# Optimization experiments

Hardware: AMD Instinct MI355X
Metric: run time of the kernel (lower is better)

Reference implementation:

```python
import jax, jax.numpy as jnp
import numpy as np

N_NODES = 50000
N_EDGES = 640000
DIM_IN = 128
DIM_OUT = 128
NUM_GRAPHS = 64


def setup_inputs() -> dict:
    key = jax.random.key(0)
    ks = jax.random.split(key, 8)
    x = jax.random.normal(ks[0], (N_NODES, DIM_IN), dtype=jnp.float32)
    edge_index = jax.random.randint(ks[1], (2, N_EDGES), 0, N_NODES, dtype=jnp.int32)
    batch = jnp.sort(jax.random.randint(ks[2], (N_NODES,), 0, NUM_GRAPHS, dtype=jnp.int32))
    s = 1.0 / np.sqrt(DIM_IN)
    W1 = jax.random.normal(ks[3], (DIM_IN, DIM_IN), dtype=jnp.float32) * s
    W2 = jax.random.normal(ks[4], (DIM_IN, DIM_IN), dtype=jnp.float32) * s
    Wlin = jax.random.normal(ks[5], (DIM_IN, DIM_OUT), dtype=jnp.float32) * s
    b1 = jnp.zeros((DIM_IN,), jnp.float32)
    b2 = jnp.zeros((DIM_IN,), jnp.float32)
    blin = jnp.zeros((DIM_OUT,), jnp.float32)
    return {"x": x, "edge_index": edge_index, "batch": batch,
            "W1": W1, "b1": b1, "W2": W2, "b2": b2, "Wlin": Wlin, "blin": blin}


def _gcn_conv(x, W, b, src, dst, n_nodes):
    # GCNConv: symmetric norm with self-loops: D^{-1/2}(A+I)D^{-1/2} X W + b
    h = x @ W                                                   # [N, d]
    deg = jax.ops.segment_sum(jnp.ones_like(dst, jnp.float32), dst,
                              num_segments=n_nodes) + 1.0       # +1 self loop
    dinv = jax.lax.rsqrt(deg)                                   # [N]
    w = dinv[src] * dinv[dst]                                   # per-edge norm [E]
    agg = jax.ops.segment_sum(h[src] * w[:, None], dst, num_segments=n_nodes)
    return agg + h * (dinv * dinv)[:, None] + b                 # self-loop term + bias


def reference(x, edge_index, batch, W1, b1, W2, b2, Wlin, blin):
    n = x.shape[0]
    src, dst = edge_index[0], edge_index[1]
    h = jax.nn.relu(_gcn_conv(x, W1, b1, src, dst, n))          # dropout = identity (eval)
    h = _gcn_conv(h, W2, b2, src, dst, n)
    # global mean pool over graphs
    s = jax.ops.segment_sum(h, batch, num_segments=NUM_GRAPHS)  # [G, d]
    cnt = jax.ops.segment_sum(jnp.ones((n,), jnp.float32), batch, num_segments=NUM_GRAPHS)
    pooled = s / jnp.maximum(cnt, 1.0)[:, None]
    return jax.nn.relu(pooled @ Wlin + blin)
```

## Files before the change

kernel.cpp:

```cpp
#include <hip/hip_runtime.h>

#define N_NODES   50000
#define N_EDGES   640000
#define DIM       128
#define NUM_GRAPHS 64
#define SLOTS     64
#define GEMM1_BLOCKS 196
#define FILL_BLOCKS  157

typedef __attribute__((ext_vector_type(8))) short          s16x8;
typedef __attribute__((ext_vector_type(8))) unsigned short u16x8;
typedef __attribute__((ext_vector_type(4))) float          f32x4;

__device__ inline float bf2f(unsigned short u) {
    unsigned v = ((unsigned)u) << 16;
    float f;
    __builtin_memcpy(&f, &v, 4);
    return f;
}
__device__ inline unsigned short f2bf(float f) {
    unsigned u;
    __builtin_memcpy(&u, &f, 4);
    u = (u + 0x7fffu + ((u >> 16) & 1u)) >> 16;
    return (unsigned short)u;
}

__global__ __launch_bounds__(128) void k_prep_w(const float* __restrict__ W1,
                                                const float* __restrict__ W2,
                                                unsigned short* __restrict__ Wt1,
                                                unsigned short* __restrict__ Wt2,
                                                int* __restrict__ cnt,
                                                float* __restrict__ pooled) {
    int k = blockIdx.x & 127;
    const float*    W  = (blockIdx.x < DIM) ? W1 : W2;
    unsigned short* Wt = (blockIdx.x < DIM) ? Wt1 : Wt2;
    int n = threadIdx.x;
    Wt[n * DIM + k] = f2bf(W[k * DIM + n]);

    int gid = blockIdx.x * 128 + threadIdx.x;
    for (int i = gid; i < N_NODES; i += 32768) cnt[i] = 0;
    if (gid < NUM_GRAPHS * DIM) pooled[gid] = 0.f;
}

__global__ __launch_bounds__(512) void k_fill_gemm1(const int* __restrict__ src,
                                                    const int* __restrict__ dst,
                                                    int* __restrict__ cnt,
                                                    unsigned short* __restrict__ slots,
                                                    const float* __restrict__ x,
                                                    const unsigned short* __restrict__ Wt1,
                                                    unsigned short* __restrict__ H1) {
    __shared__ unsigned short wsh[DIM][136];
    const int tid = threadIdx.x;

    if (blockIdx.x >= GEMM1_BLOCKS) {
        int e0 = (((blockIdx.x - GEMM1_BLOCKS) * 512) + tid) * 8;
        #pragma unroll
        for (int h = 0; h < 2; h++) {
            int e = e0 + h * 4;
            if (e + 3 < N_EDGES) {
                int4 s4 = *reinterpret_cast<const int4*>(src + e);
                int4 d4 = *reinterpret_cast<const int4*>(dst + e);
                int p0 = atomicAdd(&cnt[d4.x], 1);
                int p1 = atomicAdd(&cnt[d4.y], 1);
                int p2 = atomicAdd(&cnt[d4.z], 1);
                int p3 = atomicAdd(&cnt[d4.w], 1);
                if (p0 < SLOTS) slots[d4.x * SLOTS + p0] = (unsigned short)s4.x;
                if (p1 < SLOTS) slots[d4.y * SLOTS + p1] = (unsigned short)s4.y;
                if (p2 < SLOTS) slots[d4.z * SLOTS + p2] = (unsigned short)s4.z;
                if (p3 < SLOTS) slots[d4.w * SLOTS + p3] = (unsigned short)s4.w;
            } else if (e < N_EDGES) {
                for (int q = e; q < N_EDGES; q++) {
                    int s = src[q], d = dst[q];
                    int p = atomicAdd(&cnt[d], 1);
                    if (p < SLOTS) slots[d * SLOTS + p] = (unsigned short)s;
                }
            }
        }
        return;
    }

    #pragma unroll
    for (int i = 0; i < 4; i++) {
        int off = tid * 8 + i * 4096;
        int r = off >> 7, cc = off & 127;
        u16x8 v = *reinterpret_cast<const u16x8*>(Wt1 + off);
        *reinterpret_cast<u16x8*>(&wsh[r][cc]) = v;
    }
    __syncthreads();

    const int wid  = tid >> 6;
    const int lane = tid & 63;
    const int l15  = lane & 15;
    const int lk   = lane >> 4;
    const int row0 = blockIdx.x * 256 + wid * 32;

    f32x4 acc[2][8];
    #pragma unroll
    for (int a = 0; a < 2; a++)
        #pragma unroll
        for (int n = 0; n < 8; n++) acc[a][n] = (f32x4){0.f, 0.f, 0.f, 0.f};

    const long long r0 = min(row0 + l15,      N_NODES - 1);
    const long long r1 = min(row0 + 16 + l15, N_NODES - 1);

    #pragma unroll
    for (int kk = 0; kk < 4; kk++) {
        const int kb = kk * 32 + lk * 8;
        s16x8 a0, a1;
        const float4 p0 = *reinterpret_cast<const float4*>(x + r0 * DIM + kb);
        const float4 q0 = *reinterpret_cast<const float4*>(x + r0 * DIM + kb + 4);
        const float4 p1 = *reinterpret_cast<const float4*>(x + r1 * DIM + kb);
        const float4 q1 = *reinterpret_cast<const float4*>(x + r1 * DIM + kb + 4);
        a0[0]=(short)f2bf(p0.x); a0[1]=(short)f2bf(p0.y); a0[2]=(short)f2bf(p0.z); a0[3]=(short)f2bf(p0.w);
        a0[4]=(short)f2bf(q0.x); a0[5]=(short)f2bf(q0.y); a0[6]=(short)f2bf(q0.z); a0[7]=(short)f2bf(q0.w);
        a1[0]=(short)f2bf(p1.x); a1[1]=(short)f2bf(p1.y); a1[2]=(short)f2bf(p1.z); a1[3]=(short)f2bf(p1.w);
        a1[4]=(short)f2bf(q1.x); a1[5]=(short)f2bf(q1.y); a1[6]=(short)f2bf(q1.z); a1[7]=(short)f2bf(q1.w);
        #pragma unroll
        for (int n = 0; n < 8; n++) {
            s16x8 b = *reinterpret_cast<const s16x8*>(&wsh[n * 16 + l15][kb]);
            acc[0][n] = __builtin_amdgcn_mfma_f32_16x16x32_bf16(a0, b, acc[0][n], 0, 0, 0);
            acc[1][n] = __builtin_amdgcn_mfma_f32_16x16x32_bf16(a1, b, acc[1][n], 0, 0, 0);
        }
    }

    #pragma unroll
    for (int rh = 0; rh < 2; rh++) {
        #pragma unroll
        for (int j = 0; j < 4; j++) {
            int row = row0 + rh * 16 + lk * 4 + j;
            if (row < N_NODES) {
                #pragma unroll
                for (int n = 0; n < 8; n++)
                    H1[(long long)row * DIM + n * 16 + l15] = f2bf(acc[rh][n][j]);
            }
        }
    }
}

__global__ __launch_bounds__(512) void k_gemm2(const unsigned short* __restrict__ Ab,
                                               const unsigned short* __restrict__ Wt,
                                               unsigned short* __restrict__ H) {
    __shared__ unsigned short wsh[DIM][136];
    const int tid = threadIdx.x;

    #pragma unroll
    for (int i = 0; i < 4; i++) {
        int off = tid * 8 + i * 4096;
        int r = off >> 7, cc = off & 127;
        u16x8 v = *reinterpret_cast<const u16x8*>(Wt + off);
        *reinterpret_cast<u16x8*>(&wsh[r][cc]) = v;
    }
    __syncthreads();

    const int wid  = tid >> 6;
    const int lane = tid & 63;
    const int l15  = lane & 15;
    const int lk   = lane >> 4;
    const int row0 = blockIdx.x * 256 + wid * 32;

    f32x4 acc[2][8];
    #pragma unroll
    for (int a = 0; a < 2; a++)
        #pragma unroll
        for (int n = 0; n < 8; n++) acc[a][n] = (f32x4){0.f, 0.f, 0.f, 0.f};

    const long long r0 = min(row0 + l15,      N_NODES - 1);
    const long long r1 = min(row0 + 16 + l15, N_NODES - 1);

    #pragma unroll
    for (int kk = 0; kk < 4; kk++) {
        const int kb = kk * 32 + lk * 8;
        s16x8 a0 = *reinterpret_cast<const s16x8*>(Ab + r0 * DIM + kb);
        s16x8 a1 = *reinterpret_cast<const s16x8*>(Ab + r1 * DIM + kb);
        #pragma unroll
        for (int n = 0; n < 8; n++) {
            s16x8 b = *reinterpret_cast<const s16x8*>(&wsh[n * 16 + l15][kb]);
            acc[0][n] = __builtin_amdgcn_mfma_f32_16x16x32_bf16(a0, b, acc[0][n], 0, 0, 0);
            acc[1][n] = __builtin_amdgcn_mfma_f32_16x16x32_bf16(a1, b, acc[1][n], 0, 0, 0);
        }
    }

    #pragma unroll
    for (int rh = 0; rh < 2; rh++) {
        #pragma unroll
        for (int j = 0; j < 4; j++) {
            int row = row0 + rh * 16 + lk * 4 + j;
            if (row < N_NODES) {
                #pragma unroll
                for (int n = 0; n < 8; n++)
                    H[(long long)row * DIM + n * 16 + l15] = f2bf(acc[rh][n][j]);
            }
        }
    }
}

__device__ inline void gather_node(const int* __restrict__ cnt,
                                   const unsigned short* __restrict__ slots,
                                   const unsigned short* __restrict__ h,
                                   const float* __restrict__ bias,
                                   int n, int c, float dn, float* acc) {
    float d2 = dn * dn;
    u16x8 hv = *reinterpret_cast<const u16x8*>(h + (size_t)n * DIM + c);
    #pragma unroll
    for (int j = 0; j < 8; j++) acc[j] = bf2f(hv[j]) * d2 + bias[c + j];

    const int m = min(cnt[n], SLOTS);
    const unsigned short* sl = slots + (size_t)n * SLOTS;

    int i = 0;
    for (; i + 3 < m; i += 4) {
        int s0 = sl[i], s1 = sl[i + 1], s2 = sl[i + 2], s3 = sl[i + 3];
        float w0 = rsqrtf((float)cnt[s0] + 1.0f) * dn;
        float w1 = rsqrtf((float)cnt[s1] + 1.0f) * dn;
        float w2 = rsqrtf((float)cnt[s2] + 1.0f) * dn;
        float w3 = rsqrtf((float)cnt[s3] + 1.0f) * dn;
        u16x8 v0 = *reinterpret_cast<const u16x8*>(h + (size_t)s0 * DIM + c);
        u16x8 v1 = *reinterpret_cast<const u16x8*>(h + (size_t)s1 * DIM + c);
        u16x8 v2 = *reinterpret_cast<const u16x8*>(h + (size_t)s2 * DIM + c);
        u16x8 v3 = *reinterpret_cast<const u16x8*>(h + (size_t)s3 * DIM + c);
        #pragma unroll
        for (int j = 0; j < 8; j++)
            acc[j] += (bf2f(v0[j]) * w0 + bf2f(v1[j]) * w1) +
                      (bf2f(v2[j]) * w2 + bf2f(v3[j]) * w3);
    }
    for (; i < m; i++) {
        int s0 = sl[i];
        float w0 = rsqrtf((float)cnt[s0] + 1.0f) * dn;
        u16x8 v0 = *reinterpret_cast<const u16x8*>(h + (size_t)s0 * DIM + c);
        #pragma unroll
        for (int j = 0; j < 8; j++) acc[j] += bf2f(v0[j]) * w0;
    }
}

__global__ __launch_bounds__(256) void k_pull1(const int* __restrict__ cnt,
                                               const unsigned short* __restrict__ slots,
                                               const unsigned short* __restrict__ h,
                                               const float* __restrict__ bias,
                                               unsigned short* __restrict__ outp) {
    int gid = blockIdx.x * blockDim.x + threadIdx.x;
    int n = gid >> 4;
    if (n >= N_NODES) return;
    int c = (gid & 15) << 3;

    float dn = rsqrtf((float)cnt[n] + 1.0f);
    float acc[8];
    gather_node(cnt, slots, h, bias, n, c, dn, acc);

    u16x8 o;
    #pragma unroll
    for (int j = 0; j < 8; j++) o[j] = f2bf(fmaxf(acc[j], 0.f));
    *reinterpret_cast<u16x8*>(outp + (size_t)n * DIM + c) = o;
}

__global__ __launch_bounds__(256) void k_pull_pool(const int* __restrict__ cnt,
                                                   const unsigned short* __restrict__ slots,
                                                   const unsigned short* __restrict__ h,
                                                   const float* __restrict__ bias,
                                                   const int* __restrict__ batch,
                                                   float* __restrict__ pooled) {
    __shared__ float pool_l[2][DIM];
    const int tid  = threadIdx.x;
    const int base = blockIdx.x * 64;
    const int c    = (tid & 15) << 3;

    pool_l[tid >> 7][tid & 127] = 0.f;
    __syncthreads();

    const int gmin = batch[min(base, N_NODES - 1)];

    #pragma unroll
    for (int r = 0; r < 4; r++) {
        int n = base + r * 16 + (tid >> 4);
        bool valid = n < N_NODES;
        int nn = min(n, N_NODES - 1);

        float dn = rsqrtf((float)cnt[nn] + 1.0f);
        float acc[8];
        gather_node(cnt, slots, h, bias, nn, c, dn, acc);
        if (!valid) {
            #pragma unroll
            for (int j = 0; j < 8; j++) acc[j] = 0.f;
        }

        const int g = batch[nn];
        const int d = g - gmin;

        if (__all(g == __shfl(g, 0))) {
            #pragma unroll
            for (int j = 0; j < 8; j++) {
                acc[j] += __shfl_xor(acc[j], 16);
                acc[j] += __shfl_xor(acc[j], 32);
            }
            if ((tid & 63) < 16) {
                if (d < 2) {
                    #pragma unroll
                    for (int j = 0; j < 8; j++) atomicAdd(&pool_l[d][c + j], acc[j]);
                } else {
                    #pragma unroll
                    for (int j = 0; j < 8; j++) atomicAdd(&pooled[g * DIM + c + j], acc[j]);
                }
            }
        } else {
            if (d < 2) {
                #pragma unroll
                for (int j = 0; j < 8; j++) atomicAdd(&pool_l[d][c + j], acc[j]);
            } else {
                #pragma unroll
                for (int j = 0; j < 8; j++) atomicAdd(&pooled[g * DIM + c + j], acc[j]);
            }
        }
    }
    __syncthreads();

    const int f = tid & 127;
    if (tid < 128) {
        atomicAdd(&pooled[gmin * DIM + f], pool_l[0][f]);
    } else {
        int last = min(base + 63, N_NODES - 1);
        if (batch[last] > gmin) atomicAdd(&pooled[(gmin + 1) * DIM + f], pool_l[1][f]);
    }
}

__global__ __launch_bounds__(128) void k_pool2(const float* __restrict__ pooled,
                                               const int* __restrict__ batch,
                                               const float* __restrict__ Wlin,
                                               const float* __restrict__ blin,
                                               float* __restrict__ out) {
    int g = blockIdx.x;
    int t = threadIdx.x;
    __shared__ int se[2];
    __shared__ float pr[DIM];
    if (t < 2) {
        int target = g + t;
        int lo = 0, hi = N_NODES;
        while (lo < hi) { int mid = (lo + hi) >> 1; if (batch[mid] < target) lo = mid + 1; else hi = mid; }
        se[t] = lo;
    }
    __syncthreads();
    float inv_cnt = 1.0f / fmaxf((float)(se[1] - se[0]), 1.0f);
    pr[t] = pooled[g * DIM + t] * inv_cnt;
    __syncthreads();
    float acc = blin[t];
    #pragma unroll 8
    for (int k = 0; k < DIM; k++) acc += pr[k] * Wlin[k * DIM + t];
    out[g * DIM + t] = fmaxf(acc, 0.f);
}

extern "C" void kernel_launch(void* const* d_in, const int* in_sizes, int n_in,
                              void* d_out, int out_size, void* d_ws, size_t ws_size,
                              hipStream_t stream) {
    const float* x          = (const float*)d_in[0];
    const int*   edge_index = (const int*)d_in[1];
    const int*   batch      = (const int*)d_in[2];
    const float* W1         = (const float*)d_in[3];
    const float* b1         = (const float*)d_in[4];
    const float* W2         = (const float*)d_in[5];
    const float* b2         = (const float*)d_in[6];
    const float* Wlin       = (const float*)d_in[7];
    const float* blin       = (const float*)d_in[8];
    float*       out        = (float*)d_out;

    const int* src = edge_index;
    const int* dst = edge_index + N_EDGES;

    char* ws = (char*)d_ws;
    size_t off = 0;
    auto alloc = [&](size_t bytes) { void* p = ws + off; off = (off + bytes + 255) & ~255ULL; return p; };
    int*            cnt    = (int*)            alloc((size_t)N_NODES * 4);
    unsigned short* slots  = (unsigned short*) alloc((size_t)N_NODES * SLOTS * 2);
    float*          pooled = (float*)          alloc((size_t)NUM_GRAPHS * DIM * 4);
    unsigned short* Wt1    = (unsigned short*) alloc((size_t)DIM * DIM * 2);
    unsigned short* Wt2    = (unsigned short*) alloc((size_t)DIM * DIM * 2);
    unsigned short* H1     = (unsigned short*) alloc((size_t)N_NODES * DIM * 2);
    unsigned short* Z1     = (unsigned short*) alloc((size_t)N_NODES * DIM * 2);
    unsigned short* H2     = (unsigned short*) alloc((size_t)N_NODES * DIM * 2);

    const int pull1Blocks = (N_NODES * 16 + 255) / 256;
    const int poolBlocks  = (N_NODES + 63) / 64;
    const int gemmBlocks  = (N_NODES + 255) / 256;

    k_prep_w<<<2 * DIM, DIM, 0, stream>>>(W1, W2, Wt1, Wt2, cnt, pooled);

    k_fill_gemm1<<<GEMM1_BLOCKS + FILL_BLOCKS, 512, 0, stream>>>(src, dst, cnt, slots, x, Wt1, H1);

    k_pull1<<<pull1Blocks, 256, 0, stream>>>(cnt, slots, H1, b1, Z1);

    k_gemm2<<<gemmBlocks, 512, 0, stream>>>(Z1, Wt2, H2);

    k_pull_pool<<<poolBlocks, 256, 0, stream>>>(cnt, slots, H2, b2, batch, pooled);

    k_pool2<<<NUM_GRAPHS, 128, 0, stream>>>(pooled, batch, Wlin, blin, out);
}
```

Baseline: 122.2 us.

## Move second GCN weight multiply after aggregation and pooling via linearity

Because the second conv's weight multiply is linear, aggregation and mean pooling are applied to Z1 directly, and W2 and b2 are applied only to the 64 pooled rows in the final kernel. This drops the 50000x128x128 second GEMM, the H2 buffer write and read, and one kernel launch. The trade-off is changed rounding: the aggregation now runs on bf16 Z1 instead of bf16 H2, and W2 is applied in fp32 on pooled values.

```diff
diff --git a/kernel.cpp b/kernel.cpp
--- a/kernel.cpp
+++ b/kernel.cpp
@@ -26,19 +26,15 @@
 }
 
 __global__ __launch_bounds__(128) void k_prep_w(const float* __restrict__ W1,
-                                                const float* __restrict__ W2,
                                                 unsigned short* __restrict__ Wt1,
-                                                unsigned short* __restrict__ Wt2,
                                                 int* __restrict__ cnt,
                                                 float* __restrict__ pooled) {
-    int k = blockIdx.x & 127;
-    const float*    W  = (blockIdx.x < DIM) ? W1 : W2;
-    unsigned short* Wt = (blockIdx.x < DIM) ? Wt1 : Wt2;
+    int k = blockIdx.x;
     int n = threadIdx.x;
-    Wt[n * DIM + k] = f2bf(W[k * DIM + n]);
+    Wt1[n * DIM + k] = f2bf(W1[k * DIM + n]);
 
     int gid = blockIdx.x * 128 + threadIdx.x;
-    for (int i = gid; i < N_NODES; i += 32768) cnt[i] = 0;
+    for (int i = gid; i < N_NODES; i += 16384) cnt[i] = 0;
     if (gid < NUM_GRAPHS * DIM) pooled[gid] = 0.f;
 }
 
@@ -137,63 +133,7 @@
     }
 }
 
-__global__ __launch_bounds__(512) void k_gemm2(const unsigned short* __restrict__ Ab,
-                                               const unsigned short* __restrict__ Wt,
-                                               unsigned short* __restrict__ H) {
-    __shared__ unsigned short wsh[DIM][136];
-    const int tid = threadIdx.x;
-
-    #pragma unroll
-    for (int i = 0; i < 4; i++) {
-        int off = tid * 8 + i * 4096;
-        int r = off >> 7, cc = off & 127;
-        u16x8 v = *reinterpret_cast<const u16x8*>(Wt + off);
-        *reinterpret_cast<u16x8*>(&wsh[r][cc]) = v;
-    }
-    __syncthreads();
-
-    const int wid  = tid >> 6;
-    const int lane = tid & 63;
-    const int l15  = lane & 15;
-    const int lk   = lane >> 4;
-    const int row0 = blockIdx.x * 256 + wid * 32;
-
-    f32x4 acc[2][8];
-    #pragma unroll
-    for (int a = 0; a < 2; a++)
-        #pragma unroll
-        for (int n = 0; n < 8; n++) acc[a][n] = (f32x4){0.f, 0.f, 0.f, 0.f};
-
-    const long long r0 = min(row0 + l15,      N_NODES - 1);
-    const long long r1 = min(row0 + 16 + l15, N_NODES - 1);
-
-    #pragma unroll
-    for (int kk = 0; kk < 4; kk++) {
-        const int kb = kk * 32 + lk * 8;
-        s16x8 a0 = *reinterpret_cast<const s16x8*>(Ab + r0 * DIM + kb);
-        s16x8 a1 = *reinterpret_cast<const s16x8*>(Ab + r1 * DIM + kb);
-        #pragma unroll
-        for (int n = 0; n < 8; n++) {
-            s16x8 b = *reinterpret_cast<const s16x8*>(&wsh[n * 16 + l15][kb]);
-            acc[0][n] = __builtin_amdgcn_mfma_f32_16x16x32_bf16(a0, b, acc[0][n], 0, 0, 0);
-            acc[1][n] = __builtin_amdgcn_mfma_f32_16x16x32_bf16(a1, b, acc[1][n], 0, 0, 0);
-        }
-    }
-
-    #pragma unroll
-    for (int rh = 0; rh < 2; rh++) {
-        #pragma unroll
-        for (int j = 0; j < 4; j++) {
-            int row = row0 + rh * 16 + lk * 4 + j;
-            if (row < N_NODES) {
-                #pragma unroll
-                for (int n = 0; n < 8; n++)
-                    H[(long long)row * DIM + n * 16 + l15] = f2bf(acc[rh][n][j]);
-            }
-        }
-    }
-}
-
+template<int WITH_BIAS>
 __device__ inline void gather_node(const int* __restrict__ cnt,
                                    const unsigned short* __restrict__ slots,
                                    const unsigned short* __restrict__ h,
@@ -202,7 +142,7 @@
     float d2 = dn * dn;
     u16x8 hv = *reinterpret_cast<const u16x8*>(h + (size_t)n * DIM + c);
     #pragma unroll
-    for (int j = 0; j < 8; j++) acc[j] = bf2f(hv[j]) * d2 + bias[c + j];
+    for (int j = 0; j < 8; j++) acc[j] = bf2f(hv[j]) * d2 + (WITH_BIAS ? bias[c + j] : 0.f);
 
     const int m = min(cnt[n], SLOTS);
     const unsigned short* sl = slots + (size_t)n * SLOTS;
@@ -244,7 +184,7 @@
 
     float dn = rsqrtf((float)cnt[n] + 1.0f);
     float acc[8];
-    gather_node(cnt, slots, h, bias, n, c, dn, acc);
+    gather_node<1>(cnt, slots, h, bias, n, c, dn, acc);
 
     u16x8 o;
     #pragma unroll
@@ -255,7 +195,6 @@
 __global__ __launch_bounds__(256) void k_pull_pool(const int* __restrict__ cnt,
                                                    const unsigned short* __restrict__ slots,
                                                    const unsigned short* __restrict__ h,
-                                                   const float* __restrict__ bias,
                                                    const int* __restrict__ batch,
                                                    float* __restrict__ pooled) {
     __shared__ float pool_l[2][DIM];
@@ -276,7 +215,7 @@
 
         float dn = rsqrtf((float)cnt[nn] + 1.0f);
         float acc[8];
-        gather_node(cnt, slots, h, bias, nn, c, dn, acc);
+        gather_node<0>(cnt, slots, h, nullptr, nn, c, dn, acc);
         if (!valid) {
             #pragma unroll
             for (int j = 0; j < 8; j++) acc[j] = 0.f;
@@ -321,15 +260,18 @@
     }
 }
 
-__global__ __launch_bounds__(128) void k_pool2(const float* __restrict__ pooled,
+__global__ __launch_bounds__(128) void k_pool2(const float* __restrict__ pooledA,
                                                const int* __restrict__ batch,
+                                               const float* __restrict__ W2,
+                                               const float* __restrict__ b2,
                                                const float* __restrict__ Wlin,
                                                const float* __restrict__ blin,
                                                float* __restrict__ out) {
     int g = blockIdx.x;
     int t = threadIdx.x;
     __shared__ int se[2];
-    __shared__ float pr[DIM];
+    __shared__ float pa[DIM];
+    __shared__ float z[DIM];
     if (t < 2) {
         int target = g + t;
         int lo = 0, hi = N_NODES;
@@ -338,12 +280,17 @@
     }
     __syncthreads();
     float inv_cnt = 1.0f / fmaxf((float)(se[1] - se[0]), 1.0f);
-    pr[t] = pooled[g * DIM + t] * inv_cnt;
-    __syncthreads();
-    float acc = blin[t];
+    pa[t] = pooledA[g * DIM + t] * inv_cnt;
+    __syncthreads();
+    float acc = b2[t];
     #pragma unroll 8
-    for (int k = 0; k < DIM; k++) acc += pr[k] * Wlin[k * DIM + t];
-    out[g * DIM + t] = fmaxf(acc, 0.f);
+    for (int k = 0; k < DIM; k++) acc += pa[k] * W2[k * DIM + t];
+    z[t] = acc;
+    __syncthreads();
+    float acc2 = blin[t];
+    #pragma unroll 8
+    for (int k = 0; k < DIM; k++) acc2 += z[k] * Wlin[k * DIM + t];
+    out[g * DIM + t] = fmaxf(acc2, 0.f);
 }
 
 extern "C" void kernel_launch(void* const* d_in, const int* in_sizes, int n_in,
@@ -370,24 +317,19 @@
     unsigned short* slots  = (unsigned short*) alloc((size_t)N_NODES * SLOTS * 2);
     float*          pooled = (float*)          alloc((size_t)NUM_GRAPHS * DIM * 4);
     unsigned short* Wt1    = (unsigned short*) alloc((size_t)DIM * DIM * 2);
-    unsigned short* Wt2    = (unsigned short*) alloc((size_t)DIM * DIM * 2);
     unsigned short* H1     = (unsigned short*) alloc((size_t)N_NODES * DIM * 2);
     unsigned short* Z1     = (unsigned short*) alloc((size_t)N_NODES * DIM * 2);
-    unsigned short* H2     = (unsigned short*) alloc((size_t)N_NODES * DIM * 2);
 
     const int pull1Blocks = (N_NODES * 16 + 255) / 256;
     const int poolBlocks  = (N_NODES + 63) / 64;
-    const int gemmBlocks  = (N_NODES + 255) / 256;
-
-    k_prep_w<<<2 * DIM, DIM, 0, stream>>>(W1, W2, Wt1, Wt2, cnt, pooled);
+
+    k_prep_w<<<DIM, DIM, 0, stream>>>(W1, Wt1, cnt, pooled);
 
     k_fill_gemm1<<<GEMM1_BLOCKS + FILL_BLOCKS, 512, 0, stream>>>(src, dst, cnt, slots, x, Wt1, H1);
 
     k_pull1<<<pull1Blocks, 256, 0, stream>>>(cnt, slots, H1, b1, Z1);
 
-    k_gemm2<<<gemmBlocks, 512, 0, stream>>>(Z1, Wt2, H2);
-
-    k_pull_pool<<<poolBlocks, 256, 0, stream>>>(cnt, slots, H2, b2, batch, pooled);
-
-    k_pool2<<<NUM_GRAPHS, 128, 0, stream>>>(pooled, batch, Wlin, blin, out);
-}
+    k_pull_pool<<<poolBlocks, 256, 0, stream>>>(cnt, slots, Z1, batch, pooled);
+
+    k_pool2<<<NUM_GRAPHS, 128, 0, stream>>>(pooled, batch, W2, b2, Wlin, blin, out);
+}
```

Measured after the change: 119.2 us. 2.4% less time.
